# Kernel optimization log

Measured on AMD Instinct MI355X. Metric: run time of the kernel, lower is better.

## Reference

```python
import jax, jax.numpy as jnp
import numpy as np

K = 3        # kernel_size
EPS = 1e-4   # eps from __init__


def _conv_valid(x, w):
    # NHWC input, HWIO filter, VALID padding, stride 1
    return jax.lax.conv_general_dilated(
        x, w, window_strides=(1, 1), padding='VALID',
        dimension_numbers=('NHWC', 'HWIO', 'NHWC'))


def _backward_standardize_weight(grad_in, original_weights, gain, w_max_bitmap, eps):
    # Faithful translation of BackwardInjectWSConv2D.backward_standardize_weight
    kh, kw, cin, cout = original_weights.shape
    N = float(kh * kw * cin)                       # b*h*w in the TF code
    mu = jnp.mean(original_weights, axis=(0, 1, 2))
    xmu = original_weights - mu                    # [K,K,Cin,Cout]
    var = jnp.mean(jnp.square(xmu), axis=(0, 1, 2))
    mvar = N * var
    maxvar = jnp.maximum(mvar, eps)
    sqrtvar = jnp.sqrt(maxvar)
    ivar = 1.0 / sqrtvar
    givar = gain * ivar                            # [Cout]
    dgivar = jnp.sum(grad_in * xmu, axis=(0, 1, 2))
    divar = dgivar * gain
    dgain = dgivar * ivar
    dxmu1 = grad_in * givar
    dsqrtvar = (-1.0 / jnp.square(sqrtvar)) * divar
    dmaxvar = (0.5 / jnp.sqrt(maxvar)) * dsqrtvar
    dmvar = w_max_bitmap * dmaxvar
    dvar = N * dmvar
    dsq = (1.0 / N) * dvar                         # (1/N)*ones_like(grad_in)*dvar, broadcast
    dxmu2 = 2.0 * xmu * dsq
    dx1 = dxmu1 + dxmu2
    dmu = -jnp.sum(dx1, axis=(0, 1, 2))
    dx2 = (1.0 / N) * dmu                          # broadcast over [K,K,Cin]
    dx = dx1 + dx2
    return dx, dgain


def setup_inputs() -> dict:
    key = jax.random.key(0)
    ks = jax.random.split(key, 5)
    B, H, W, Cin, Cout = 64, 56, 56, 128, 128
    return {
        'grad_output': jax.random.normal(ks[0], (B, H, W, Cout), jnp.float32),
        'inputs': jax.random.normal(ks[1], (B, H, W, Cin), jnp.float32),
        'kernels': jax.random.normal(ks[2], (K, K, Cin, Cout), jnp.float32),
        'std_kernels': jax.random.normal(ks[3], (K, K, Cin, Cout), jnp.float32),
        'gain': jax.random.uniform(ks[4], (Cout,), jnp.float32),
        'w_max_bitmap': jnp.ones((Cout,), jnp.float32),
    }


def reference(grad_output, inputs, kernels, std_kernels, gain, w_max_bitmap):
    pad = (K - 1) // 2
    # ---- grad wrt input: full conv of grad_out with rot180(std_kernels), io swapped
    go_pad = jnp.pad(grad_output, ((0, 0), (pad, pad), (pad, pad), (0, 0)))
    w_rot = jnp.transpose(std_kernels[::-1, ::-1], (0, 1, 3, 2))   # [K,K,Cout,Cin]
    manual_grad_in = _conv_valid(go_pad, w_rot)                    # [B,H,W,Cin]
    # ---- grad wrt weight: treat Cin as batch, B as contraction channel
    in_pad = jnp.pad(inputs, ((0, 0), (pad, pad), (pad, pad), (0, 0)))
    fmt_inp = jnp.transpose(in_pad, (3, 1, 2, 0))                  # [Cin,H+2p,W+2p,B]
    fmt_wt = jnp.transpose(grad_output, (1, 2, 0, 3))              # [H,W,B,Cout]
    direct = _conv_valid(fmt_inp, fmt_wt)                          # [Cin,K,K,Cout]
    grad_wt_raw = jnp.transpose(direct, (1, 2, 0, 3))              # [K,K,Cin,Cout]
    # ---- weight-standardization backward chain
    manual_grad_wt, manual_grad_gain = _backward_standardize_weight(
        grad_wt_raw, kernels, gain, w_max_bitmap, EPS)
    # ---- bias grad
    manual_grad_bias = jnp.sum(grad_output, axis=(0, 1, 2))        # [Cout]
    return manual_grad_in, manual_grad_wt, manual_grad_bias, manual_grad_gain
```

## Files before the change

### kernel.cpp

```cpp
#include <hip/hip_runtime.h>
#include <hip/hip_bf16.h>

typedef __bf16 bf16x8 __attribute__((ext_vector_type(8)));
typedef __bf16 bf16x4 __attribute__((ext_vector_type(4)));
typedef float  f32x4  __attribute__((ext_vector_type(4)));
typedef unsigned int u32;

#define HW_   3136
#define NPIX  200704
#define GI_ELEMS 25690112

#define GOT_OFF   0u
#define RAW_OFF   51380224u
#define BIASA_OFF 51970048u
#define STDKF_OFF 51970560u
#define GUARD_OFF 52265472u
#define ZB_OFF    52265728u
#define ZA_OFF    52272000u
#define X_OFF     52279168u

__device__ __forceinline__ f32x4 mfma16(bf16x8 a, bf16x8 b, f32x4 c){
  return __builtin_amdgcn_mfma_f32_16x16x32_bf16(a, b, c, 0, 0, 0);
}

__device__ __forceinline__ void async16(const void* g, __bf16* l){
  __builtin_amdgcn_global_load_lds(
      (const __attribute__((address_space(1))) void*)g,
      (__attribute__((address_space(3))) void*)l, 16, 0, 0);
}

__global__ __launch_bounds__(256) void k_prep(const float* __restrict__ s, __bf16* __restrict__ d){
  const int g = blockIdx.x*256 + threadIdx.x;
  const int l = g & 63;
  const int j = (g >> 6) & 7;
  const int kc = (g >> 9) & 3;
  const int tap = g >> 11;
  const int ci = j*16 + (l & 15);
  const int co0 = kc*32 + (l >> 4)*8;
  const float* src = s + ((size_t)(tap*128 + ci))*128 + co0;
  f32x4 x0 = *(const f32x4*)src;
  f32x4 x1 = *(const f32x4*)(src + 4);
  bf16x8 y;
  #pragma unroll
  for (int e=0;e<4;e++){ y[e] = (__bf16)x0[e]; y[e+4] = (__bf16)x1[e]; }
  *(bf16x8*)(d + (size_t)g*8) = y;
}

__global__ __launch_bounds__(256) void k_goT(const float* __restrict__ go,
                                             __bf16* __restrict__ goT,
                                             __bf16* __restrict__ goB,
                                             float* __restrict__ biasA){
  __shared__ __bf16 T[64][130];
  __shared__ float biasS[128];
  const int t = threadIdx.x;
  const size_t p0 = (size_t)blockIdx.x*64;
  if (t < 128) biasS[t] = 0.f;
  __syncthreads();
  float bs[4] = {0.f,0.f,0.f,0.f};
  const int co0 = (t*4) & 127;
  #pragma unroll
  for (int i=0;i<8;i++){
    const int flat = (i*256+t)*4;
    const int px = flat >> 7, co = flat & 127;
    f32x4 x = *(const f32x4*)(go + p0*128 + flat);
    bf16x4 y;
    #pragma unroll
    for (int e=0;e<4;e++){ y[e] = (__bf16)x[e]; bs[e] += x[e]; }
    *(bf16x4*)&T[px][co] = y;
    *(bf16x4*)(goB + p0*128 + flat) = y;
  }
  #pragma unroll
  for (int e=0;e<4;e++) atomicAdd(&biasS[co0+e], bs[e]);
  __syncthreads();
  #pragma unroll
  for (int j=0;j<2;j++){
    const int task = j*256 + t;
    const int co = task >> 2, q = task & 3;
    bf16x8 v0, v1;
    #pragma unroll
    for (int k=0;k<8;k++) v0[k] = T[q*16+k][co];
    #pragma unroll
    for (int k=0;k<8;k++) v1[k] = T[q*16+8+k][co];
    __bf16* d = goT + (size_t)co*NPIX + p0 + q*16;
    *(bf16x8*)d = v0; *(bf16x8*)(d+8) = v1;
  }
  if (t < 128) atomicAdd(&biasA[t], biasS[t]);
}

__global__ __launch_bounds__(256) void k_inT(const float* __restrict__ inp,
                                             __bf16* __restrict__ inT){
  __shared__ __bf16 T[64][130];
  const int t = threadIdx.x;
  const size_t p0 = (size_t)blockIdx.x*64;
  #pragma unroll
  for (int i=0;i<8;i++){
    const int flat = (i*256+t)*4;
    const int px = flat >> 7, ci = flat & 127;
    f32x4 x = *(const f32x4*)(inp + p0*128 + flat);
    bf16x4 y;
    #pragma unroll
    for (int e=0;e<4;e++) y[e] = (__bf16)x[e];
    *(bf16x4*)&T[px][ci] = y;
  }
  __syncthreads();
  #pragma unroll
  for (int j=0;j<4;j++){
    const int task = j*256 + t;
    const int ci = task >> 3, ch = task & 7;
    const int p = (int)p0 + ch*8;
    const int b = p / HW_; const int r = p - b*HW_;
    const int h = r / 56;  const int w = r - h*56;
    bf16x8 v;
    #pragma unroll
    for (int k=0;k<8;k++) v[k] = T[ch*8+k][ci];
    *(bf16x8*)(inT + (((size_t)(ci*64+b))*58 + (h+1))*64 + w) = v;
  }
}

__global__ __launch_bounds__(256) void k_padz(__bf16* __restrict__ inT){
  const int g = blockIdx.x*256 + threadIdx.x;
  const int pair = g / 72, k = g - pair*72;
  __bf16* base = inT + (size_t)pair*3712;
  int off;
  if (k < 8)       off = k*8;
  else if (k < 16) off = 57*64 + (k-8)*8;
  else             off = (k-15)*64 + 56;
  bf16x8 z = {};
  *(bf16x8*)(base + off) = z;
}

__global__ __launch_bounds__(512, 2) void k_gradin5(const __bf16* __restrict__ goB,
                                                    const __bf16* __restrict__ stdkF,
                                                    const __bf16* __restrict__ zsrc,
                                                    float* __restrict__ out){
  __shared__ char LDS[74240];
  const int t = threadIdx.x;
  const int wv = t >> 6, l = t & 63, lr = l & 15, lg = l >> 4;
  const int b = blockIdx.x, h0 = blockIdx.y*8;
  const int j0 = (wv & 1)*4;
  const int pxg = (wv >> 1)*112;

  int sb[7];
  #pragma unroll
  for (int tile=0; tile<7; ++tile){
    const int p = pxg + tile*16 + lr;
    const int ro = p / 56; const int w = p - ro*56;
    sb[tile] = (ro + 2)*58 + (w + 2);
  }

  f32x4 acc[7][4];
  #pragma unroll
  for (int i=0;i<7;i++){
    #pragma unroll
    for (int j=0;j<4;j++){
      #pragma unroll
      for (int r=0;r<4;r++) acc[i][j][r] = 0.f;
    }
  }

  for (int c=0; c<2; ++c){
    #pragma unroll
    for (int it=0; it<10; ++it){
      const int qb = it*512 + wv*64;
      const u32 q = (u32)(qb + l);
      if (q < 4640u){
        const u32 r = q / 464u;
        const u32 rem = q - r*464u;
        const u32 wp = rem >> 3;
        const u32 cl = rem & 7u;
        const int h = h0 - 1 + (int)r;
        const u32 s = r*58u + wp;
        const u32 csrc = cl ^ (s & 7u);
        const bool valid = (h >= 0) & (h < 56) & (wp >= 1u) & (wp <= 56u);
        const __bf16* src = valid
          ? goB + ((size_t)((b*HW_) + h*56 + ((int)wp - 1))*128 + c*64 + csrc*8)
          : zsrc;
        async16(src, (__bf16*)(LDS + qb*16));
      }
    }
    __syncthreads();

    for (int tap=0; tap<9; ++tap){
      const int u = tap/3;
      const int soff = u*58 + (tap - u*3);
      #pragma unroll
      for (int kc=0; kc<2; ++kc){
        const int kcg = c*2 + kc;
        bf16x8 Bf[4];
        #pragma unroll
        for (int j=0;j<4;++j)
          Bf[j] = *(const bf16x8*)(stdkF + ((size_t)(((tap*4 + kcg)*8 + j0 + j)*64 + l))*8);
        bf16x8 Af[7];
        #pragma unroll
        for (int tile=0;tile<7;++tile){
          const int s = sb[tile] - soff;
          const int byte = (s << 7) | (((kc*4 + lg) ^ (s & 7)) << 4);
          Af[tile] = *(const bf16x8*)(LDS + byte);
        }
        #pragma unroll
        for (int tile=0;tile<7;++tile){
          #pragma unroll
          for (int j=0;j<4;++j)
            acc[tile][j] = mfma16(Af[tile], Bf[j], acc[tile][j]);
        }
      }
    }
    __syncthreads();
  }

  float* o = out + ((size_t)b*HW_ + (size_t)h0*56 + pxg)*128;
  #pragma unroll
  for (int tile=0;tile<7;++tile){
    #pragma unroll
    for (int j=0;j<4;++j){
      #pragma unroll
      for (int r=0;r<4;++r)
        o[(size_t)(tile*16 + 4*lg + r)*128 + (j0 + j)*16 + lr] = acc[tile][j][r];
    }
  }
}

#define GW_G 29696
#define GW_A 29728

#define KSTEP(ks)                                                              \
{                                                                              \
  const int pl = (ks)*32 + lg*8;                                               \
  const int q  = (ks)*4 + lg;                                                  \
  const int hl = q / 7;                                                        \
  const int w0 = pl - hl*56;                                                   \
  bf16x8 b0 = *(const bf16x8*)&LDS[(wco + lr)*232 + pl];                       \
  bf16x8 b1 = *(const bf16x8*)&LDS[(wco + 16 + lr)*232 + pl];                  \
  const __bf16* abase = &LDS[GW_A + lr*392 + hl*64 + w0];                      \
  _Pragma("unroll")                                                            \
  for (int u=0; u<3; ++u){                                                     \
    const __bf16* ap = abase + u*64;                                           \
    union { bf16x8 v; u32 d[4]; } vp, va, vn, a0, a2;                          \
    vp.v = *(const bf16x8*)(ap - 8);                                           \
    va.v = *(const bf16x8*)ap;                                                 \
    vn.v = *(const bf16x8*)(ap + 8);                                           \
    a0.d[0] = (va.d[0] << 16) | (vp.d[3] >> 16);                               \
    a0.d[1] = (va.d[1] << 16) | (va.d[0] >> 16);                               \
    a0.d[2] = (va.d[2] << 16) | (va.d[1] >> 16);                               \
    a0.d[3] = (va.d[3] << 16) | (va.d[2] >> 16);                               \
    a2.d[0] = (va.d[0] >> 16) | (va.d[1] << 16);                               \
    a2.d[1] = (va.d[1] >> 16) | (va.d[2] << 16);                               \
    a2.d[2] = (va.d[2] >> 16) | (va.d[3] << 16);                               \
    a2.d[3] = (va.d[3] >> 16) | (vn.d[0] << 16);                               \
    acc[u*3+0][0] = mfma16(a0.v, b0, acc[u*3+0][0]);                           \
    acc[u*3+0][1] = mfma16(a0.v, b1, acc[u*3+0][1]);                           \
    acc[u*3+1][0] = mfma16(va.v, b0, acc[u*3+1][0]);                           \
    acc[u*3+1][1] = mfma16(va.v, b1, acc[u*3+1][1]);                           \
    acc[u*3+2][0] = mfma16(a2.v, b0, acc[u*3+2][0]);                           \
    acc[u*3+2][1] = mfma16(a2.v, b1, acc[u*3+2][1]);                           \
  }                                                                            \
}

__global__ __launch_bounds__(256, 2) void k_gradwt7(const char* __restrict__ ws,
                                                    float* __restrict__ raw){
  __shared__ __bf16 LDS[36000];
  const int t = threadIdx.x;
  const int w = t >> 6, l = t & 63, lr = l & 15, lg = l >> 4;
  const int b = blockIdx.x, ci0 = blockIdx.y*16;
  const int wco = w*32;

  if (t < 32) LDS[GW_G + t] = (__bf16)0.f;

  u32 boff[15];
  #pragma unroll
  for (int i=0;i<15;i++){
    const int chunk = i*256 + w*64 + l;
    if (chunk < 3712){
      const int co = chunk / 29, part = chunk - co*29;
      boff[i] = (part < 28)
        ? (GOT_OFF + (u32)(co*NPIX + b*HW_ + part*8)*2u)
        : ZB_OFF;
    } else boff[i] = ZB_OFF;
  }
  u32 aoff[4];
  #pragma unroll
  for (int i=0;i<4;i++){
    const int chunk = i*256 + w*64 + l;
    if (chunk < 784){
      const int ci = chunk / 49, r = chunk - ci*49;
      aoff[i] = (r < 48)
        ? (X_OFF + (u32)((((ci0+ci)*64 + b)*58 + (r>>3))*64 + (r&7)*8)*2u)
        : ZA_OFF;
    } else aoff[i] = ZA_OFF;
  }

  f32x4 acc[9][2];
  #pragma unroll
  for (int tp=0;tp<9;tp++){
    #pragma unroll
    for (int j=0;j<2;j++){
      #pragma unroll
      for (int r=0;r<4;r++) acc[tp][j][r] = 0.f;
    }
  }

  for (int c=0; c<14; ++c){
    #pragma unroll
    for (int i=0;i<15;i++){
      if (i < 14 || w < 2){
        async16(ws + boff[i], LDS + (i*256 + w*64)*8);
        boff[i] += 448u;
      }
    }
    #pragma unroll
    for (int i=0;i<4;i++){
      const int chunk = i*256 + w*64 + l;
      if (chunk < 784){
        async16(ws + aoff[i], LDS + GW_A + (i*256 + w*64)*8);
        aoff[i] += 512u;
      }
    }
    __syncthreads();

    KSTEP(0) KSTEP(1) KSTEP(2) KSTEP(3) KSTEP(4) KSTEP(5) KSTEP(6)

    __syncthreads();
  }

  #pragma unroll
  for (int tp=0;tp<9;tp++){
    #pragma unroll
    for (int j=0;j<2;j++){
      #pragma unroll
      for (int r=0;r<4;r++)
        atomicAdd(&raw[(size_t)(tp*128 + ci0 + 4*lg + r)*128 + wco + j*16 + lr],
                  acc[tp][j][r]);
    }
  }
}

__global__ __launch_bounds__(128) void k_std(const float* __restrict__ raw,
      const float* __restrict__ kern, const float* __restrict__ gain,
      const float* __restrict__ bmap, const float* __restrict__ biasA,
      float* __restrict__ out_wt, float* __restrict__ out_bias, float* __restrict__ out_gain){
  const int co = blockIdx.x, t = threadIdx.x;
  float kv[9], gv[9];
  float s1=0.f, s2=0.f, sg=0.f, sgk=0.f;
  #pragma unroll
  for (int i=0;i<9;i++){
    const int m = t + i*128;
    const float k_ = kern[(size_t)m*128 + co];
    const float g_ = raw [(size_t)m*128 + co];
    kv[i]=k_; gv[i]=g_;
    s1 += k_; s2 += k_*k_; sg += g_; sgk += g_*k_;
  }
  __shared__ float red[4][128];
  red[0][t]=s1; red[1][t]=s2; red[2][t]=sg; red[3][t]=sgk;
  __syncthreads();
  for (int off=64; off>0; off>>=1){
    if (t < off){
      red[0][t]+=red[0][t+off]; red[1][t]+=red[1][t+off];
      red[2][t]+=red[2][t+off]; red[3][t]+=red[3][t+off];
    }
    __syncthreads();
  }
  const float N = 1152.f;
  const float S1=red[0][0], S2=red[1][0], Sg=red[2][0], Sgk=red[3][0];
  const float mu = S1/N;
  const float var = S2/N - mu*mu;
  const float mvar = N*var;
  const float maxvar = fmaxf(mvar, 1e-4f);
  const float sqrtvar = sqrtf(maxvar);
  const float ivar = 1.f/sqrtvar;
  const float g = gain[co];
  const float givar = g*ivar;
  const float dgivar = Sgk - mu*Sg;
  const float divar = dgivar*g;
  const float dsqrtvar = -divar/maxvar;
  const float dmaxvar = 0.5f*dsqrtvar/sqrtvar;
  const float dsq = bmap[co]*dmaxvar;
  const float dmu = -(givar*Sg + 2.f*dsq*(S1 - N*mu));
  const float dmuN = dmu*(1.f/N);
  #pragma unroll
  for (int i=0;i<9;i++){
    const int m = t + i*128;
    out_wt[(size_t)m*128 + co] = gv[i]*givar + 2.f*(kv[i]-mu)*dsq + dmuN;
  }
  if (t == 0){ out_gain[co] = dgivar*ivar; out_bias[co] = biasA[co]; }
}

extern "C" void kernel_launch(void* const* d_in, const int* in_sizes, int n_in,
                              void* d_out, int out_size, void* d_ws, size_t ws_size,
                              hipStream_t stream){
  const float* go   = (const float*)d_in[0];
  const float* inp  = (const float*)d_in[1];
  const float* kern = (const float*)d_in[2];
  const float* stdk = (const float*)d_in[3];
  const float* gain = (const float*)d_in[4];
  const float* bmap = (const float*)d_in[5];

  char* ws = (char*)d_ws;
  __bf16* goT   = (__bf16*)(ws + GOT_OFF);
  float*  raw   = (float*) (ws + RAW_OFF);
  float*  biasA = (float*) (ws + BIASA_OFF);
  __bf16* stdkF = (__bf16*)(ws + STDKF_OFF);
  char*   guard =           ws + GUARD_OFF;
  __bf16* goB   = (__bf16*)(ws + X_OFF);
  __bf16* inT   = (__bf16*)(ws + X_OFF);

  hipMemsetAsync(ws + RAW_OFF,   0, 589824 + 512, stream);
  hipMemsetAsync(ws + GUARD_OFF, 0, 256 + 6272 + 7168, stream);

  k_prep  <<<72, 256, 0, stream>>>(stdk, stdkF);
  k_goT   <<<3136, 256, 0, stream>>>(go, goT, goB, biasA);
  k_gradin5<<<dim3(64,7), 512, 0, stream>>>(goB, stdkF, (const __bf16*)guard, (float*)d_out);

  k_padz  <<<2304, 256, 0, stream>>>(inT);
  k_inT   <<<3136, 256, 0, stream>>>(inp, inT);
  k_gradwt7<<<dim3(64,8), 256, 0, stream>>>((const char*)ws, raw);

  float* out = (float*)d_out;
  k_std<<<128, 128, 0, stream>>>(raw, kern, gain, bmap, biasA,
                                 out + GI_ELEMS,
                                 out + GI_ELEMS + 147456,
                                 out + GI_ELEMS + 147456 + 128);
}
```

Measured before the change: 300.7 us.

## Double-buffer gradwt LDS tiles and fold pad-zeroing into input transpose

The weight-gradient kernel now loads half-size chunks (two image rows instead of four) into two alternating LDS buffers. The next chunk's async copy is issued before the MFMA work on the current one, replacing the old load-sync-compute-sync loop. The last k-step is masked with zeros because the chunk width no longer divides evenly. The separate pad-zeroing kernel is merged into the input-transpose kernel to save a launch. The cost is more loop iterations, extra masking logic and larger LDS use, which may limit occupancy.

```diff
diff --git a/kernel.cpp b/kernel.cpp
--- a/kernel.cpp
+++ b/kernel.cpp
@@ -92,6 +92,19 @@
   __shared__ __bf16 T[64][130];
   const int t = threadIdx.x;
   const size_t p0 = (size_t)blockIdx.x*64;
+
+  if (blockIdx.x < 2304){
+    const int g = blockIdx.x*256 + t;
+    const int pair = g / 72, k = g - pair*72;
+    __bf16* base = inT + (size_t)pair*3712;
+    int off;
+    if (k < 8)       off = k*8;
+    else if (k < 16) off = 57*64 + (k-8)*8;
+    else             off = (k-15)*64 + 56;
+    bf16x8 z = {};
+    *(bf16x8*)(base + off) = z;
+  }
+
   #pragma unroll
   for (int i=0;i<8;i++){
     const int flat = (i*256+t)*4;
@@ -115,18 +128,6 @@
     for (int k=0;k<8;k++) v[k] = T[ch*8+k][ci];
     *(bf16x8*)(inT + (((size_t)(ci*64+b))*58 + (h+1))*64 + w) = v;
   }
-}
-
-__global__ __launch_bounds__(256) void k_padz(__bf16* __restrict__ inT){
-  const int g = blockIdx.x*256 + threadIdx.x;
-  const int pair = g / 72, k = g - pair*72;
-  __bf16* base = inT + (size_t)pair*3712;
-  int off;
-  if (k < 8)       off = k*8;
-  else if (k < 16) off = 57*64 + (k-8)*8;
-  else             off = (k-15)*64 + 56;
-  bf16x8 z = {};
-  *(bf16x8*)(base + off) = z;
 }
 
 __global__ __launch_bounds__(512, 2) void k_gradin5(const __bf16* __restrict__ goB,
@@ -220,18 +221,16 @@
   }
 }
 
-#define GW_G 29696
-#define GW_A 29728
-
-#define KSTEP(ks)                                                              \
+#define KSTEP9(ks)                                                             \
 {                                                                              \
   const int pl = (ks)*32 + lg*8;                                               \
   const int q  = (ks)*4 + lg;                                                  \
   const int hl = q / 7;                                                        \
   const int w0 = pl - hl*56;                                                   \
-  bf16x8 b0 = *(const bf16x8*)&LDS[(wco + lr)*232 + pl];                       \
-  bf16x8 b1 = *(const bf16x8*)&LDS[(wco + 16 + lr)*232 + pl];                  \
-  const __bf16* abase = &LDS[GW_A + lr*392 + hl*64 + w0];                      \
+  const int plc = ((ks)==3 && lg==3) ? 112 : pl;                               \
+  bf16x8 b0 = *(const bf16x8*)&Bb[(wco + lr)*120 + plc];                       \
+  bf16x8 b1 = *(const bf16x8*)&Bb[(wco + 16 + lr)*120 + plc];                  \
+  const __bf16* abase = &Ab[lr*264 + hl*64 + w0];                              \
   _Pragma("unroll")                                                            \
   for (int u=0; u<3; ++u){                                                     \
     const __bf16* ap = abase + u*64;                                           \
@@ -239,6 +238,11 @@
     vp.v = *(const bf16x8*)(ap - 8);                                           \
     va.v = *(const bf16x8*)ap;                                                 \
     vn.v = *(const bf16x8*)(ap + 8);                                           \
+    if ((ks)==3 && lg >= 2){                                                   \
+      vp.d[0]=0u; vp.d[1]=0u; vp.d[2]=0u; vp.d[3]=0u;                          \
+      va.d[0]=0u; va.d[1]=0u; va.d[2]=0u; va.d[3]=0u;                          \
+      vn.d[0]=0u; vn.d[1]=0u; vn.d[2]=0u; vn.d[3]=0u;                          \
+    }                                                                          \
     a0.d[0] = (va.d[0] << 16) | (vp.d[3] >> 16);                               \
     a0.d[1] = (va.d[1] << 16) | (va.d[0] >> 16);                               \
     a0.d[2] = (va.d[2] << 16) | (va.d[1] >> 16);                               \
@@ -256,34 +260,37 @@
   }                                                                            \
 }
 
-__global__ __launch_bounds__(256, 2) void k_gradwt7(const char* __restrict__ ws,
+__global__ __launch_bounds__(256, 2) void k_gradwt9(const char* __restrict__ ws,
                                                     float* __restrict__ raw){
-  __shared__ __bf16 LDS[36000];
+  __shared__ __bf16 LDS[39208];
   const int t = threadIdx.x;
   const int w = t >> 6, l = t & 63, lr = l & 15, lg = l >> 4;
   const int b = blockIdx.x, ci0 = blockIdx.y*16;
   const int wco = w*32;
 
-  if (t < 32) LDS[GW_G + t] = (__bf16)0.f;
-
-  u32 boff[15];
-  #pragma unroll
-  for (int i=0;i<15;i++){
-    const int chunk = i*256 + w*64 + l;
-    if (chunk < 3712){
-      const int co = chunk / 29, part = chunk - co*29;
-      boff[i] = (part < 28)
+  if (t < 40){
+    const int idx = (t < 8) ? (30720 + t) : ((t < 24) ? (34952 + t - 8) : (39192 + t - 24));
+    LDS[idx] = (__bf16)0.f;
+  }
+
+  u32 boff[8];
+  #pragma unroll
+  for (int i=0;i<8;i++){
+    const int chunk = i*256 + t;
+    if (chunk < 1920){
+      const int co = chunk / 15, part = chunk - co*15;
+      boff[i] = (part < 14)
         ? (GOT_OFF + (u32)(co*NPIX + b*HW_ + part*8)*2u)
         : ZB_OFF;
     } else boff[i] = ZB_OFF;
   }
-  u32 aoff[4];
-  #pragma unroll
-  for (int i=0;i<4;i++){
-    const int chunk = i*256 + w*64 + l;
-    if (chunk < 784){
-      const int ci = chunk / 49, r = chunk - ci*49;
-      aoff[i] = (r < 48)
+  u32 aoff[3];
+  #pragma unroll
+  for (int i=0;i<3;i++){
+    const int chunk = i*256 + t;
+    if (chunk < 528){
+      const int ci = chunk / 33, r = chunk - ci*33;
+      aoff[i] = (r < 32)
         ? (X_OFF + (u32)((((ci0+ci)*64 + b)*58 + (r>>3))*64 + (r&7)*8)*2u)
         : ZA_OFF;
     } else aoff[i] = ZA_OFF;
@@ -299,26 +306,37 @@
     }
   }
 
-  for (int c=0; c<14; ++c){
-    #pragma unroll
-    for (int i=0;i<15;i++){
-      if (i < 14 || w < 2){
-        async16(ws + boff[i], LDS + (i*256 + w*64)*8);
-        boff[i] += 448u;
+  #pragma unroll
+  for (int i=0;i<8;i++){
+    const int chunk = i*256 + t;
+    if (chunk < 1920){ async16(ws + boff[i], LDS + chunk*8); boff[i] += 224u; }
+  }
+  #pragma unroll
+  for (int i=0;i<3;i++){
+    const int chunk = i*256 + t;
+    if (chunk < 528){ async16(ws + aoff[i], LDS + 30728 + chunk*8); aoff[i] += 256u; }
+  }
+  __syncthreads();
+
+  for (int c=0; c<28; ++c){
+    const int cur = c & 1;
+    if (c < 27){
+      __bf16* dB = LDS + ((cur ^ 1) ? 15360 : 0);
+      __bf16* dA = LDS + ((cur ^ 1) ? 34968 : 30728);
+      #pragma unroll
+      for (int i=0;i<8;i++){
+        const int chunk = i*256 + t;
+        if (chunk < 1920){ async16(ws + boff[i], dB + chunk*8); boff[i] += 224u; }
       }
-    }
-    #pragma unroll
-    for (int i=0;i<4;i++){
-      const int chunk = i*256 + w*64 + l;
-      if (chunk < 784){
-        async16(ws + aoff[i], LDS + GW_A + (i*256 + w*64)*8);
-        aoff[i] += 512u;
+      #pragma unroll
+      for (int i=0;i<3;i++){
+        const int chunk = i*256 + t;
+        if (chunk < 528){ async16(ws + aoff[i], dA + chunk*8); aoff[i] += 256u; }
       }
     }
-    __syncthreads();
-
-    KSTEP(0) KSTEP(1) KSTEP(2) KSTEP(3) KSTEP(4) KSTEP(5) KSTEP(6)
-
+    const __bf16* Bb = LDS + (cur ? 15360 : 0);
+    const __bf16* Ab = LDS + (cur ? 34968 : 30728);
+    KSTEP9(0) KSTEP9(1) KSTEP9(2) KSTEP9(3)
     __syncthreads();
   }
 
@@ -410,9 +428,8 @@
   k_goT   <<<3136, 256, 0, stream>>>(go, goT, goB, biasA);
   k_gradin5<<<dim3(64,7), 512, 0, stream>>>(goB, stdkF, (const __bf16*)guard, (float*)d_out);
 
-  k_padz  <<<2304, 256, 0, stream>>>(inT);
   k_inT   <<<3136, 256, 0, stream>>>(inp, inT);
-  k_gradwt7<<<dim3(64,8), 256, 0, stream>>>((const char*)ws, raw);
+  k_gradwt9<<<dim3(64,8), 256, 0, stream>>>((const char*)ws, raw);
 
   float* out = (float*)d_out;
   k_std<<<128, 128, 0, stream>>>(raw, kern, gain, bmap, biasA,
```

Result: no change. 300.5 us (-0.1%).
